# Kernel tuning notes

Measured on AMD Instinct MI355X. Metric: run time of the kernel, lower is better.

Reference implementation:

```python
import jax, jax.numpy as jnp
import numpy as np

NUM_HEADS = 12
TOPK = 4


def setup_inputs() -> dict:
    key = jax.random.key(0)
    ks = jax.random.split(key, 5)
    B, N, C = 32, 577, 768
    s = 0.02
    return {
        "x": jax.random.normal(ks[0], (B, N, C), jnp.float32),
        "qkv_w": jax.random.normal(ks[1], (3 * C, C), jnp.float32) * s,
        "qkv_b": jax.random.normal(ks[2], (3 * C,), jnp.float32) * s,
        "proj_w": jax.random.normal(ks[3], (C, C), jnp.float32) * s,
        "proj_b": jax.random.normal(ks[4], (C,), jnp.float32) * s,
    }


def reference(x, qkv_w, qkv_b, proj_w, proj_b):
    B, N, C = x.shape
    H = NUM_HEADS
    D = C // H
    scale = D ** -0.5  # 0.125, matches original_attention.scale

    # qkv projection: (B,N,3C) -> (3,B,H,N,D)
    qkv = (x @ qkv_w.T + qkv_b).reshape(B, N, 3, H, D).transpose(2, 0, 3, 1, 4)
    q, k, v = qkv[0], qkv[1], qkv[2]

    # heuristic head routing: mean squared query energy per head
    scores = jnp.mean(q.astype(jnp.float32) ** 2, axis=(0, 2, 3))  # (H,)
    _, idx = jax.lax.top_k(scores, TOPK)
    idx = jnp.sort(idx)  # (topk,)

    q_sel = q[:, idx]  # (B,topk,N,D)
    k_sel = k[:, idx]
    v_sel = v[:, idx]

    attn = jax.nn.softmax(jnp.einsum('bhnd,bhmd->bhnm', q_sel, k_sel) * scale, axis=-1)
    y_sel = jnp.einsum('bhnm,bhmd->bhnd', attn, v_sel)  # (B,topk,N,D)

    # scatter selected heads back into full-size tensors (as in the torch module)
    y_full = jnp.zeros((B, H, N, D), x.dtype).at[:, idx].set(y_sel)
    x_out = y_full.transpose(0, 2, 1, 3).reshape(B, N, C) @ proj_w.T + proj_b

    attn_full = jnp.zeros((B, H, N, N), x.dtype).at[:, idx].set(attn)
    return x_out, attn_full
```

## Files before the change

kernel.cpp:

```cpp
#include <hip/hip_runtime.h>
#include <hip/hip_bf16.h>
#include <stdint.h>
#include <stddef.h>

#define B_ 32
#define N_ 577
#define C_ 768
#define H_ 12
#define D_ 64
#define M_ (B_*N_)
#define K3_ (3*C_)
#define NP_ 640
#define NN_ (N_*N_)

typedef __bf16 bf16x8_t __attribute__((ext_vector_type(8)));
typedef float f32x4 __attribute__((ext_vector_type(4)));
typedef unsigned short u16x8 __attribute__((ext_vector_type(8)));
typedef unsigned short u16x4 __attribute__((ext_vector_type(4)));

static __device__ __forceinline__ f32x4 mfma16(u16x8 a, u16x8 b, f32x4 c) {
  return __builtin_amdgcn_mfma_f32_16x16x32_bf16(
      __builtin_bit_cast(bf16x8_t, a), __builtin_bit_cast(bf16x8_t, b), c, 0, 0, 0);
}

static __device__ __forceinline__ unsigned short f2bf(float x) {
  unsigned int u = __builtin_bit_cast(unsigned int, x);
  u += 0x7fffu + ((u >> 16) & 1u);
  return (unsigned short)(u >> 16);
}

static __device__ __forceinline__ void glds16(const unsigned short* g, unsigned short* l) {
  __builtin_amdgcn_global_load_lds(
      (__attribute__((address_space(1))) void*)g,
      (__attribute__((address_space(3))) void*)l,
      16, 0, 0);
}

static __device__ __forceinline__ void top4sel(const float* __restrict__ scores, int* sel) {
  float s[H_];
  #pragma unroll
  for (int i = 0; i < H_; ++i) s[i] = scores[i];
  #pragma unroll
  for (int t = 0; t < 4; ++t) {
    int best = 0; float bv = s[0];
    #pragma unroll
    for (int i = 1; i < H_; ++i)
      if (s[i] > bv) { bv = s[i]; best = i; }
    sel[t] = best;
    #pragma unroll
    for (int i = 0; i < H_; ++i)
      s[i] = (i == best) ? -3.0e38f : s[i];
  }
  #pragma unroll
  for (int a = 0; a < 4; ++a)
    #pragma unroll
    for (int b2 = a + 1; b2 < 4; ++b2)
      if (sel[b2] < sel[a]) { int t = sel[a]; sel[a] = sel[b2]; sel[b2] = t; }
}

__global__ void k_cvt2(const float* __restrict__ srcx, unsigned short* __restrict__ dstx, int n4x,
                       const float* __restrict__ srcw, unsigned short* __restrict__ dstw, int n4w,
                       float* __restrict__ zeroptr) {
  if (blockIdx.x == 0 && threadIdx.x < 16) zeroptr[threadIdx.x] = 0.f;
  const float* src; unsigned short* dst; int n4, i0, stride;
  if (blockIdx.x < 2048) {
    src = srcx; dst = dstx; n4 = n4x;
    i0 = blockIdx.x * 256 + threadIdx.x; stride = 2048 * 256;
  } else {
    src = srcw; dst = dstw; n4 = n4w;
    i0 = (blockIdx.x - 2048) * 256 + threadIdx.x; stride = 512 * 256;
  }
  for (int i = i0; i < n4; i += stride) {
    float4 v = ((const float4*)src)[i];
    u16x4 o;
    o[0] = f2bf(v.x); o[1] = f2bf(v.y); o[2] = f2bf(v.z); o[3] = f2bf(v.w);
    *(u16x4*)(dst + (size_t)i * 4) = o;
  }
}

#define ZPER_ 146948
template<int MODE>
__global__ void k_gemm(const unsigned short* __restrict__ A,
                       const unsigned short* __restrict__ Bm,
                       const float* __restrict__ bias,
                       unsigned short* __restrict__ qb,
                       unsigned short* __restrict__ kb,
                       unsigned short* __restrict__ vb,
                       float* __restrict__ scores,
                       float* __restrict__ out,
                       int Mtot, int Ktot)
{
  __shared__ unsigned short As[128 * 32];
  __shared__ unsigned short Bs[128 * 32];
  const int tid = threadIdx.x;
  int bn;

  if (MODE == 0) {
    const int y = blockIdx.y;
    if ((y & 3) == 0) {
      const int zblk = (y >> 2) * 145 + blockIdx.x;
      const size_t Z = (size_t)B_ * H_ * NN_;
      size_t s0 = (size_t)zblk * ZPER_;
      size_t len = ZPER_;
      if (s0 + len > Z) len = Z - s0;
      float* zo = out + s0;
      const float4 z4 = {0.f, 0.f, 0.f, 0.f};
      for (size_t t = tid * 4; t + 4 <= len; t += 4096)
        *(float4*)(zo + t) = z4;
      return;
    }
    bn = y - 1 - (y >> 2);
  } else {
    bn = blockIdx.y;
  }

  const int bm = blockIdx.x;
  const int w = tid >> 6, l = tid & 63;
  const int wm = w >> 1, wn = w & 1;
  const int lr = l & 15, lg = l >> 4;
  const int lk = lg * 8;
  f32x4 acc[4][4] = {};
  const int rowA0 = bm * 128, rowB0 = bn * 128;
  const int le0 = w * 1024 + l * 8;
  const int kiters = Ktot >> 5;
  for (int kt = 0; kt < kiters; ++kt) {
    __syncthreads();
    #pragma unroll
    for (int c = 0; c < 2; ++c) {
      int lea = le0 + c * 512;
      int ra = lea >> 5, ka = lea & 31;
      glds16(A  + (size_t)(rowA0 + ra) * Ktot + kt * 32 + ka, As + (w * 2 + c) * 512);
      glds16(Bm + (size_t)(rowB0 + ra) * Ktot + kt * 32 + ka, Bs + (w * 2 + c) * 512);
    }
    __syncthreads();
    u16x8 af[4], bfr[4];
    #pragma unroll
    for (int i = 0; i < 4; ++i)
      af[i] = *(const u16x8*)(As + (wm * 64 + i * 16 + lr) * 32 + lk);
    #pragma unroll
    for (int j = 0; j < 4; ++j)
      bfr[j] = *(const u16x8*)(Bs + (wn * 64 + j * 16 + lr) * 32 + lk);
    #pragma unroll
    for (int i = 0; i < 4; ++i)
      #pragma unroll
      for (int j = 0; j < 4; ++j)
        acc[i][j] = mfma16(af[i], bfr[j], acc[i][j]);
  }

  const int rbase = lg * 4;
  if (MODE == 0) {
    const int n0 = rowB0 + wn * 64;
    const int t0 = n0 / C_;
    const int h0 = (n0 % C_) >> 6;
    unsigned short* dstbuf = (t0 == 0) ? qb : ((t0 == 1) ? kb : vb);
    float bs[4];
    #pragma unroll
    for (int j = 0; j < 4; ++j) bs[j] = bias[n0 + j * 16 + lr];
    float sq = 0.f;
    #pragma unroll
    for (int i = 0; i < 4; ++i) {
      const int mbase = rowA0 + wm * 64 + i * 16 + rbase;
      const int bb0 = mbase / N_;
      const int np0 = mbase - bb0 * N_;
      #pragma unroll
      for (int r = 0; r < 4; ++r) {
        const int mm = mbase + r;
        if (mm < Mtot) {
          int np = np0 + r, bb = bb0;
          if (np >= N_) { np -= N_; bb += 1; }
          unsigned short* drow = dstbuf + (((size_t)(bb * H_ + h0)) * N_ + np) * D_;
          #pragma unroll
          for (int j = 0; j < 4; ++j) {
            const float v = acc[i][j][r] + bs[j];
            if (t0 == 0) sq += v * v;
            drow[j * 16 + lr] = f2bf(v);
          }
        }
      }
    }
    if (t0 == 0) {
      #pragma unroll
      for (int s2 = 1; s2 < 64; s2 <<= 1) sq += __shfl_xor(sq, s2);
      if (l == 0) atomicAdd(scores + h0, sq);
    }
  } else {
    #pragma unroll
    for (int j = 0; j < 4; ++j) {
      const int n = rowB0 + wn * 64 + j * 16 + lr;
      const float bsj = bias[n];
      #pragma unroll
      for (int i = 0; i < 4; ++i) {
        const int mbase = rowA0 + wm * 64 + i * 16 + rbase;
        #pragma unroll
        for (int r = 0; r < 4; ++r) {
          const int mm = mbase + r;
          if (mm < Mtot) out[(size_t)mm * C_ + n] = acc[i][j][r] + bsj;
        }
      }
    }
  }
}

__global__ void k_prep(const unsigned short* __restrict__ vb, unsigned short* __restrict__ vT,
                       const float* __restrict__ scores,
                       const float* __restrict__ pw, unsigned short* __restrict__ pwsel) {
  int sel[4];
  top4sel(scores, sel);
  const int bid = blockIdx.x;
  const int tid = threadIdx.x;

  if (bid >= 1280) {
    const int i = (bid - 1280) * 256 + tid;
    const int c = i >> 8, j = i & 255;
    const int h = sel[j >> 6], d = j & 63;
    pwsel[i] = f2bf(pw[(size_t)c * C_ + h * 64 + d]);
    return;
  }

  __shared__ unsigned short t[64][72];
  const int nt = bid % 10;
  const int p  = bid / 10;
  const int b  = p >> 2, hs = p & 3;
  const int h  = sel[hs];
  const size_t bh_src = (size_t)(b * H_ + h);
  const size_t bh_dst = (size_t)(b * 4 + hs);
  const int n0 = nt * 64;
  {
    const int r = tid >> 2, q4 = (tid & 3) * 16;
    const int n = n0 + r;
    u16x8 v0, v1;
    if (n < N_) {
      const unsigned short* src = vb + (bh_src * N_ + n) * D_ + q4;
      v0 = *(const u16x8*)(src);
      v1 = *(const u16x8*)(src + 8);
    } else {
      #pragma unroll
      for (int j = 0; j < 8; ++j) { v0[j] = 0; v1[j] = 0; }
    }
    *(u16x8*)&t[r][q4] = v0;
    *(u16x8*)&t[r][q4 + 8] = v1;
  }
  __syncthreads();
  {
    const int d = tid >> 2, nc = (tid & 3) * 16;
    u16x8 w0, w1;
    #pragma unroll
    for (int j = 0; j < 8; ++j) { w0[j] = t[nc + j][d]; w1[j] = t[nc + 8 + j][d]; }
    unsigned short* dst = vT + (bh_dst * D_ + d) * NP_ + n0 + nc;
    *(u16x8*)(dst) = w0;
    *(u16x8*)(dst + 8) = w1;
  }
}

__global__ void k_attn(const unsigned short* __restrict__ qb,
                       const unsigned short* __restrict__ kb,
                       const unsigned short* __restrict__ vT,
                       const float* __restrict__ scores,
                       float* __restrict__ attn_out,
                       unsigned short* __restrict__ ysel)
{
  __shared__ unsigned short Plds[4][16][72];
  int sel[4];
  top4sel(scores, sel);
  const int bid = blockIdx.x;

  const int qt = bid >> 7;
  const int pair = bid & 127;
  const int b  = pair >> 2;
  const int hs = pair & 3;
  const int h  = sel[hs];
  const int tid = threadIdx.x;
  const int w = tid >> 6, l = tid & 63;
  const int lr = l & 15, lg = l >> 4, lk = lg * 8;
  const float sc2 = 0.125f * 1.44269504f;

  const size_t bh = (size_t)(b * H_ + h);
  const unsigned short* qbase = qb + bh * ((size_t)N_ * D_);
  const unsigned short* kbase = kb + bh * ((size_t)N_ * D_);
  const unsigned short* vbase = vT + (size_t)(b * 4 + hs) * ((size_t)D_ * NP_);
  float* aout = attn_out + bh * (size_t)NN_;

  const int qrow = qt * 64 + w * 16 + lr;
  const int qrc = (qrow < N_) ? qrow : (N_ - 1);
  u16x8 qf0 = *(const u16x8*)(qbase + (size_t)qrc * D_ + lk);
  u16x8 qf1 = *(const u16x8*)(qbase + (size_t)qrc * D_ + 32 + lk);

  float m2[4], lsum[4];
  #pragma unroll
  for (int r = 0; r < 4; ++r) { m2[r] = -1.0e30f; lsum[r] = 0.f; }

  for (int kt = 0; kt < 10; ++kt) {
    f32x4 s[4];
    bool vc[4];
    #pragma unroll
    for (int cg = 0; cg < 4; ++cg) {
      const int kc = kt * 64 + cg * 16 + lr;
      vc[cg] = (kc < N_);
      const int kcc = vc[cg] ? kc : (N_ - 1);
      const unsigned short* kp = kbase + (size_t)kcc * D_;
      u16x8 k0 = *(const u16x8*)(kp + lk);
      u16x8 k1 = *(const u16x8*)(kp + 32 + lk);
      f32x4 a = {0.f, 0.f, 0.f, 0.f};
      __builtin_amdgcn_s_setprio(1);
      a = mfma16(qf0, k0, a);
      a = mfma16(qf1, k1, a);
      __builtin_amdgcn_s_setprio(0);
      s[cg] = a;
    }
    #pragma unroll
    for (int r = 0; r < 4; ++r) {
      float tk[4];
      float mk = -1.0e30f;
      #pragma unroll
      for (int cg = 0; cg < 4; ++cg) {
        tk[cg] = vc[cg] ? s[cg][r] * sc2 : -1.0e30f;
        mk = fmaxf(mk, tk[cg]);
      }
      const float mn = fmaxf(m2[r], mk);
      float se = 0.f;
      #pragma unroll
      for (int cg = 0; cg < 4; ++cg)
        se += exp2f(tk[cg] - mn);
      lsum[r] = lsum[r] * exp2f(m2[r] - mn) + se;
      m2[r] = mn;
    }
  }
  #pragma unroll
  for (int x = 1; x < 16; x <<= 1) {
    #pragma unroll
    for (int r = 0; r < 4; ++r) {
      const float mo = __shfl_xor(m2[r], x);
      const float lo = __shfl_xor(lsum[r], x);
      const float mn = fmaxf(m2[r], mo);
      lsum[r] = lsum[r] * exp2f(m2[r] - mn) + lo * exp2f(mo - mn);
      m2[r] = mn;
    }
  }
  float off2[4];
  #pragma unroll
  for (int r = 0; r < 4; ++r) off2[r] = m2[r] + __log2f(lsum[r]);

  f32x4 y[4] = {};
  const int orow0 = qt * 64 + w * 16 + lg * 4;

  for (int kt = 0; kt < 10; ++kt) {
    f32x4 s[4];
    bool vc[4];
    #pragma unroll
    for (int cg = 0; cg < 4; ++cg) {
      const int kc = kt * 64 + cg * 16 + lr;
      vc[cg] = (kc < N_);
      const int kcc = vc[cg] ? kc : (N_ - 1);
      const unsigned short* kp = kbase + (size_t)kcc * D_;
      u16x8 k0 = *(const u16x8*)(kp + lk);
      u16x8 k1 = *(const u16x8*)(kp + 32 + lk);
      f32x4 a = {0.f, 0.f, 0.f, 0.f};
      __builtin_amdgcn_s_setprio(1);
      a = mfma16(qf0, k0, a);
      a = mfma16(qf1, k1, a);
      __builtin_amdgcn_s_setprio(0);
      s[cg] = a;
    }
    #pragma unroll
    for (int cg = 0; cg < 4; ++cg) {
      const int kc = kt * 64 + cg * 16 + lr;
      #pragma unroll
      for (int r = 0; r < 4; ++r) {
        float p = exp2f(__builtin_fmaf(s[cg][r], sc2, -off2[r]));
        p = vc[cg] ? p : 0.f;
        const int row = orow0 + r;
        if (vc[cg] && row < N_)
          aout[(size_t)row * N_ + kc] = p;
        Plds[w][lg * 4 + r][cg * 16 + lr] = f2bf(p);
      }
    }
    u16x8 pa0 = *(const u16x8*)&Plds[w][lr][lk];
    u16x8 pa1 = *(const u16x8*)&Plds[w][lr][32 + lk];
    #pragma unroll
    for (int cg2 = 0; cg2 < 4; ++cg2) {
      const unsigned short* vp = vbase + (size_t)(cg2 * 16 + lr) * NP_ + kt * 64;
      u16x8 v0 = *(const u16x8*)(vp + lk);
      u16x8 v1 = *(const u16x8*)(vp + 32 + lk);
      __builtin_amdgcn_s_setprio(1);
      y[cg2] = mfma16(pa0, v0, y[cg2]);
      y[cg2] = mfma16(pa1, v1, y[cg2]);
      __builtin_amdgcn_s_setprio(0);
    }
  }

  #pragma unroll
  for (int cg2 = 0; cg2 < 4; ++cg2)
    #pragma unroll
    for (int r = 0; r < 4; ++r) {
      const int row = orow0 + r;
      if (row < N_)
        ysel[((size_t)(b * N_ + row)) * 256 + hs * 64 + cg2 * 16 + lr] = f2bf(y[cg2][r]);
    }
}

extern "C" void kernel_launch(void* const* d_in, const int* in_sizes, int n_in,
                              void* d_out, int out_size, void* d_ws, size_t ws_size,
                              hipStream_t stream) {
  const float* x      = (const float*)d_in[0];
  const float* qkv_w  = (const float*)d_in[1];
  const float* qkv_b  = (const float*)d_in[2];
  const float* proj_w = (const float*)d_in[3];
  const float* proj_b = (const float*)d_in[4];

  float* xout = (float*)d_out;
  float* attn_out = (float*)d_out + (size_t)M_ * C_;

  char* ws = (char*)d_ws;
  size_t o = 0;
  unsigned short* xb    = (unsigned short*)(ws + o);
  unsigned short* vT    = (unsigned short*)(ws + o);
  o += 31457280;
  unsigned short* wqkvb = (unsigned short*)(ws + o); o += 3538944;
  unsigned short* qb    = (unsigned short*)(ws + o); o += 28360704;
  unsigned short* kb    = (unsigned short*)(ws + o); o += 28360704;
  unsigned short* vb    = (unsigned short*)(ws + o); o += 28360704;
  unsigned short* ysel  = (unsigned short*)(ws + o); o += 9453568;
  unsigned short* pwsel = (unsigned short*)(ws + o); o += 393216;
  float* scores         = (float*)(ws + o);

  k_cvt2<<<2560, 256, 0, stream>>>(x, xb, (M_ * C_) / 4,
                                   qkv_w, wqkvb, (K3_ * C_) / 4, scores);

  k_gemm<0><<<dim3(145, 24), 256, 0, stream>>>(xb, wqkvb, qkv_b,
                                               qb, kb, vb, scores, attn_out,
                                               M_, C_);

  k_prep<<<2048, 256, 0, stream>>>(vb, vT, scores, proj_w, pwsel);

  k_attn<<<1280, 256, 0, stream>>>(qb, kb, vT, scores, attn_out, ysel);

  k_gemm<1><<<dim3(145, 6), 256, 0, stream>>>(ysel, pwsel, proj_b,
                                              nullptr, nullptr, nullptr, nullptr, xout,
                                              M_, 256);
}
```

Baseline: 361.7 us.

## Split QKV GEMM so zero-fill touches only unselected attention heads

Splits the fused QKV GEMM into two launches: one computes Q and the head scores, the second computes K/V and zero-fills the attention output. Because the scores are already known when the second launch runs, it zeroes only the 8 unselected heads' attn slabs instead of the whole tensor. The selected heads are left for the attention kernel to overwrite. Grids are also flattened to 1D with bn as the fast index, which may change L2 reuse. The cost is an extra launch and a serialization point between the Q pass and the K/V pass.

```diff
diff --git a/kernel.cpp b/kernel.cpp
--- a/kernel.cpp
+++ b/kernel.cpp
@@ -78,7 +78,6 @@
   }
 }
 
-#define ZPER_ 146948
 template<int MODE>
 __global__ void k_gemm(const unsigned short* __restrict__ A,
                        const unsigned short* __restrict__ Bm,
@@ -93,28 +92,45 @@
   __shared__ unsigned short As[128 * 32];
   __shared__ unsigned short Bs[128 * 32];
   const int tid = threadIdx.x;
-  int bn;
+  const int bid = blockIdx.x;
+  int bm, bn;
 
   if (MODE == 0) {
-    const int y = blockIdx.y;
-    if ((y & 3) == 0) {
-      const int zblk = (y >> 2) * 145 + blockIdx.x;
-      const size_t Z = (size_t)B_ * H_ * NN_;
-      size_t s0 = (size_t)zblk * ZPER_;
-      size_t len = ZPER_;
-      if (s0 + len > Z) len = Z - s0;
-      float* zo = out + s0;
+    bn = bid % 6;  bm = bid / 6;
+  } else if (MODE == 1) {
+    bn = bid % 6;  bm = bid / 6;
+  } else {
+    if (bid < 2048 && (bid & 3) == 0) {
+      const int z = bid >> 2;
+      const int slab = z >> 1, half = z & 1;
+      const int zb = slab >> 3, hu = slab & 7;
+      int sel[4]; top4sel(scores, sel);
+      int uh[8]; int u = 0;
+      #pragma unroll
+      for (int c = 0; c < H_; ++c) {
+        bool issel = (c == sel[0]) | (c == sel[1]) | (c == sel[2]) | (c == sel[3]);
+        if (!issel) { uh[u] = c; ++u; }
+      }
+      int zh = 0;
+      #pragma unroll
+      for (int u2 = 0; u2 < 8; ++u2) if (u2 == hu) zh = uh[u2];
+      float* zo = out + ((size_t)(zb * H_ + zh)) * NN_ + (half ? 166464 : 0);
+      size_t take = half ? (NN_ - 166464) : 166464;
+      const int mis = (int)(((uintptr_t)zo >> 2) & 3);
+      size_t head = mis ? (size_t)(4 - mis) : 0;
+      if (head > take) head = take;
+      for (size_t t = tid; t < head; t += 256) zo[t] = 0.f;
+      float* pv = zo + head; size_t nrem = take - head;
+      const size_t nv = nrem >> 2;
       const float4 z4 = {0.f, 0.f, 0.f, 0.f};
-      for (size_t t = tid * 4; t + 4 <= len; t += 4096)
-        *(float4*)(zo + t) = z4;
+      for (size_t t = tid; t < nv; t += 256) ((float4*)pv)[t] = z4;
+      for (size_t t = (nv << 2) + tid; t < nrem; t += 256) pv[t] = 0.f;
       return;
     }
-    bn = y - 1 - (y >> 2);
-  } else {
-    bn = blockIdx.y;
-  }
-
-  const int bm = blockIdx.x;
+    const int g = (bid < 2048) ? (bid - 1 - (bid >> 2)) : (1536 + (bid - 2048));
+    bn = 6 + g % 12;  bm = g / 12;
+  }
+
   const int w = tid >> 6, l = tid & 63;
   const int wm = w >> 1, wn = w & 1;
   const int lr = l & 15, lg = l >> 4;
@@ -148,11 +164,11 @@
   }
 
   const int rbase = lg * 4;
-  if (MODE == 0) {
+  if (MODE == 0 || MODE == 2) {
     const int n0 = rowB0 + wn * 64;
     const int t0 = n0 / C_;
     const int h0 = (n0 % C_) >> 6;
-    unsigned short* dstbuf = (t0 == 0) ? qb : ((t0 == 1) ? kb : vb);
+    unsigned short* dstbuf = (MODE == 0) ? qb : ((t0 == 1) ? kb : vb);
     float bs[4];
     #pragma unroll
     for (int j = 0; j < 4; ++j) bs[j] = bias[n0 + j * 16 + lr];
@@ -172,13 +188,13 @@
           #pragma unroll
           for (int j = 0; j < 4; ++j) {
             const float v = acc[i][j][r] + bs[j];
-            if (t0 == 0) sq += v * v;
+            if (MODE == 0) sq += v * v;
             drow[j * 16 + lr] = f2bf(v);
           }
         }
       }
     }
-    if (t0 == 0) {
+    if (MODE == 0) {
       #pragma unroll
       for (int s2 = 1; s2 < 64; s2 <<= 1) sq += __shfl_xor(sq, s2);
       if (l == 0) atomicAdd(scores + h0, sq);
@@ -426,15 +442,19 @@
   k_cvt2<<<2560, 256, 0, stream>>>(x, xb, (M_ * C_) / 4,
                                    qkv_w, wqkvb, (K3_ * C_) / 4, scores);
 
-  k_gemm<0><<<dim3(145, 24), 256, 0, stream>>>(xb, wqkvb, qkv_b,
-                                               qb, kb, vb, scores, attn_out,
-                                               M_, C_);
+  k_gemm<0><<<870, 256, 0, stream>>>(xb, wqkvb, qkv_b,
+                                     qb, kb, vb, scores, nullptr,
+                                     M_, C_);
+
+  k_gemm<2><<<2252, 256, 0, stream>>>(xb, wqkvb, qkv_b,
+                                      qb, kb, vb, scores, attn_out,
+                                      M_, C_);
 
   k_prep<<<2048, 256, 0, stream>>>(vb, vT, scores, proj_w, pwsel);
 
   k_attn<<<1280, 256, 0, stream>>>(qb, kb, vT, scores, attn_out, ysel);
 
-  k_gemm<1><<<dim3(145, 6), 256, 0, stream>>>(ysel, pwsel, proj_b,
-                                              nullptr, nullptr, nullptr, nullptr, xout,
-                                              M_, 256);
-}
+  k_gemm<1><<<870, 256, 0, stream>>>(ysel, pwsel, proj_b,
+                                     nullptr, nullptr, nullptr, nullptr, xout,
+                                     M_, 256);
+}
```

Result: slower. 452.2 us (+25.0%).
